# Optimization experiments

Hardware: AMD Instinct MI355X
Metric: run time of the kernel (lower is better)

The kernel has to match this reference:

```python
import jax, jax.numpy as jnp
import numpy as np

VOCAB, HIDDEN, BATCH, T = 32000, 256, 16, 256


def setup_inputs() -> dict:
    key = jax.random.key(0)
    ks = jax.random.split(key, 8)
    s_in = 1.0 / np.sqrt(HIDDEN)  # torch nn.RNN init scale (1/sqrt(hidden))
    inputs = jax.random.randint(ks[0], (BATCH, T), 0, VOCAB)
    targets = jax.random.randint(ks[1], (BATCH, T), 0, VOCAB)
    # RNN params: torch stores W_ih as (hidden, vocab); we keep the transpose
    # (vocab, hidden) so one_hot(x) @ W_ih.T == Wih[x] (an exact gather).
    Wih = jax.random.uniform(ks[2], (VOCAB, HIDDEN), minval=-s_in, maxval=s_in)
    bih = jax.random.uniform(ks[3], (HIDDEN,), minval=-s_in, maxval=s_in)
    Whh = jax.random.uniform(ks[4], (HIDDEN, HIDDEN), minval=-s_in, maxval=s_in)
    bhh = jax.random.uniform(ks[5], (HIDDEN,), minval=-s_in, maxval=s_in)
    Wfc = jax.random.uniform(ks[6], (VOCAB, HIDDEN), minval=-s_in, maxval=s_in)
    bfc = jax.random.uniform(ks[7], (VOCAB,), minval=-s_in, maxval=s_in)
    return {"inputs": inputs, "targets": targets, "Wih": Wih, "bih": bih,
            "Whh": Whh, "bhh": bhh, "Wfc": Wfc, "bfc": bfc}


def reference(inputs, targets, Wih, bih, Whh, bhh, Wfc, bfc):
    # one_hot(inputs) @ W_ih.T + b_ih  ==  Wih[inputs] + bih (exact same math)
    xproj = Wih[inputs] + bih                      # (B, T, H)
    B = inputs.shape[0]
    h0 = jnp.zeros((B, HIDDEN), dtype=Wih.dtype)

    def step(h, xt):
        h = jnp.tanh(xt + h @ Whh.T + bhh)
        return h, h

    _, hs = jax.lax.scan(step, h0, jnp.swapaxes(xproj, 0, 1))  # (T, B, H)
    hs = jnp.swapaxes(hs, 0, 1)                    # (B, T, H)
    logits = hs @ Wfc.T + bfc                      # (B, T, V)
    logp = jax.nn.log_softmax(logits, axis=-1)
    nll = -jnp.take_along_axis(logp, targets[..., None], axis=-1)
    return jnp.mean(nll)                           # scalar cross-entropy loss
```

## Files before the change

kernel.cpp:

```cpp
#include <hip/hip_runtime.h>
#include <hip/hip_bf16.h>
#include <stdint.h>

#define VOCAB 32000
#define HID   256
#define BATCH 16
#define SEQT  256
#define ROWS  (BATCH*SEQT)

typedef __attribute__((ext_vector_type(8))) short bf16x8_t;
typedef __attribute__((ext_vector_type(4))) float f32x4_t;

__device__ __forceinline__ short f2bs(float x) {
    __hip_bfloat16 h = __float2bfloat16(x);
    return *reinterpret_cast<short*>(&h);
}
__device__ __forceinline__ bf16x8_t cvt8(float4 a, float4 b) {
    union { short s[8]; bf16x8_t v; } u;
    u.s[0] = f2bs(a.x); u.s[1] = f2bs(a.y); u.s[2] = f2bs(a.z); u.s[3] = f2bs(a.w);
    u.s[4] = f2bs(b.x); u.s[5] = f2bs(b.y); u.s[6] = f2bs(b.z); u.s[7] = f2bs(b.w);
    return u.v;
}
__device__ __forceinline__ void barrier_lds() {
    asm volatile("s_waitcnt lgkmcnt(0)\n\ts_barrier" ::: "memory");
}
__device__ __forceinline__ float tanh_exp(float x) {
    float e = __builtin_amdgcn_exp2f(x * 2.885390081777927f);
    return fmaf(-2.f, __builtin_amdgcn_rcpf(e + 1.f), 1.f);
}
__device__ __forceinline__ uint32_t pk_bf16(float lo, float hi) {
    uint32_t r;
    asm("v_cvt_pk_bf16_f32 %0, %1, %2" : "=v"(r) : "v"(lo), "v"(hi));
    return r;
}

__global__ __launch_bounds__(256) void xproj_kernel(
    const int* __restrict__ inputs,
    const float* __restrict__ Wih,
    const float* __restrict__ bih,
    const float* __restrict__ bhh,
    const float* __restrict__ Wfc,
    float* __restrict__ xp,
    float* __restrict__ S,
    __hip_bfloat16* __restrict__ Wfcb,
    int do_cvt)
{
    int idx = blockIdx.x * 256 + threadIdx.x;
    int h  = idx & 255;
    int tb = idx >> 8;
    int b  = tb & 15;
    int t  = tb >> 4;
    int id = inputs[b * SEQT + t];
    xp[idx] = Wih[(size_t)id * HID + h] + bih[h] + bhh[h];
    if (idx < ROWS) S[idx] = 0.0f;
    if (do_cvt && idx < (VOCAB * HID / 8)) {
        const float4* p = (const float4*)(Wfc + (size_t)idx * 8);
        *(bf16x8_t*)((short*)Wfcb + (size_t)idx * 8) = cvt8(p[0], p[1]);
    }
}

__global__ __launch_bounds__(512, 1) void rnn_kernel(
    const float* __restrict__ xp,
    const float* __restrict__ Whh,
    __hip_bfloat16* __restrict__ hs)
{
    __shared__ short hbuf[2][16][264];
    const int tid = threadIdx.x;
    const int l = tid & 63, w = tid >> 6;
    const int lr = l & 15, lh = l >> 4;
    const int cm = tid >> 5;
    const int cc = (tid & 31) * 8;
    const int n0 = w * 32 + lr * 2;

    bf16x8_t bfrag[2][8];
#pragma unroll
    for (int nt = 0; nt < 2; nt++) {
#pragma unroll
        for (int ki = 0; ki < 8; ki++) {
            const float4* p = (const float4*)(Whh + (size_t)(n0 + nt) * HID + ki * 32 + lh * 8);
            bfrag[nt][ki] = cvt8(p[0], p[1]);
        }
    }
    for (int i = tid; i < 16 * 264; i += 512) ((short*)hbuf[0])[i] = 0;
    __syncthreads();

    float2 xva[4], xvb[4];
#pragma unroll
    for (int r = 0; r < 4; r++)
        xva[r] = *(const float2*)(xp + (lh * 4 + r) * HID + n0);

    auto step = [&](int SRC, int DST, float2* xv, float2* xn, int t) {
        if (t > 0) {
            bf16x8_t hv = *(const bf16x8_t*)(&hbuf[SRC][cm][cc]);
            *(bf16x8_t*)((short*)hs + (size_t)(t - 1) * (BATCH * HID) + cm * HID + cc) = hv;
        }
        bf16x8_t afr[8];
#pragma unroll
        for (int ki = 0; ki < 8; ki++)
            afr[ki] = *(const bf16x8_t*)(&hbuf[SRC][lr][ki * 32 + lh * 8]);

        f32x4_t a0a = {xv[0].x, xv[1].x, xv[2].x, xv[3].x};
        f32x4_t a1a = {xv[0].y, xv[1].y, xv[2].y, xv[3].y};
        f32x4_t a0b = {0.f, 0.f, 0.f, 0.f};
        f32x4_t a1b = {0.f, 0.f, 0.f, 0.f};
#pragma unroll
        for (int ki = 0; ki < 4; ki++) {
            a0a = __builtin_amdgcn_mfma_f32_16x16x32_bf16(afr[ki],     bfrag[0][ki],     a0a, 0, 0, 0);
            a0b = __builtin_amdgcn_mfma_f32_16x16x32_bf16(afr[ki + 4], bfrag[0][ki + 4], a0b, 0, 0, 0);
            a1a = __builtin_amdgcn_mfma_f32_16x16x32_bf16(afr[ki],     bfrag[1][ki],     a1a, 0, 0, 0);
            a1b = __builtin_amdgcn_mfma_f32_16x16x32_bf16(afr[ki + 4], bfrag[1][ki + 4], a1b, 0, 0, 0);
        }

        if (t + 1 < SEQT) {
            const float* xb = xp + (size_t)(t + 1) * (BATCH * HID);
#pragma unroll
            for (int r = 0; r < 4; r++)
                xn[r] = *(const float2*)(xb + (lh * 4 + r) * HID + n0);
        }

#pragma unroll
        for (int r = 0; r < 4; r++) {
            float v0 = a0a[r] + a0b[r];
            float v1 = a1a[r] + a1b[r];
            uint32_t pk = pk_bf16(tanh_exp(v0), tanh_exp(v1));
            *(uint32_t*)(&hbuf[DST][lh * 4 + r][n0]) = pk;
        }
        barrier_lds();
    };

    for (int t = 0; t < SEQT; t += 2) {
        step(0, 1, xva, xvb, t);
        step(1, 0, xvb, xva, t + 1);
    }
    bf16x8_t hv = *(const bf16x8_t*)(&hbuf[0][cm][cc]);
    *(bf16x8_t*)((short*)hs + (size_t)(SEQT - 1) * (BATCH * HID) + cm * HID + cc) = hv;
}

template <bool BF16B>
__global__ __launch_bounds__(256) void fc_kernel(
    const __hip_bfloat16* __restrict__ hs,
    const void* __restrict__ WfcP,
    const float* __restrict__ bfc,
    const int* __restrict__ targets,
    float* __restrict__ S,
    float* __restrict__ TL)
{
    __shared__ short As[2][4 * 128 * 8];
    __shared__ short Bs[2][4 * 128 * 8];
    __shared__ int tgt[128];

    const int bid = blockIdx.x;
    const int xcd = bid & 7;
    const int j   = bid >> 3;
    const int m_id = j & 31;
    const int n_id = (j >> 5) * 8 + xcd;
    if (n_id >= VOCAB / 128) return;
    const int m0 = m_id * 128, n0 = n_id * 128;

    const int tid = threadIdx.x;
    const int l = tid & 63, w = tid >> 6;
    const int lr = l & 15, lh = l >> 4;
    const int wm = (w >> 1) * 64, wn = (w & 1) * 64;
    const int row = tid & 127, sub = tid >> 7;

    if (tid < 128) {
        int r = m0 + tid;
        tgt[tid] = targets[((r & 15) << 8) | (r >> 4)];
    }

    f32x4_t acc[4][4];
    const f32x4_t z = {0.f, 0.f, 0.f, 0.f};
#pragma unroll
    for (int i = 0; i < 4; i++)
#pragma unroll
        for (int jj = 0; jj < 4; jj++) acc[i][jj] = z;

    const __hip_bfloat16* gA = hs + (size_t)(m0 + row) * HID + sub * 8;
    const __hip_bfloat16* gBb = (const __hip_bfloat16*)WfcP + (size_t)(n0 + row) * HID + sub * 8;
    const float*          gBf = (const float*)WfcP + (size_t)(n0 + row) * HID + sub * 8;

    bf16x8_t rA0, rA1, rB0, rB1;
    float4 rf0a, rf0b, rf1a, rf1b;

    {
        rA0 = *(const bf16x8_t*)(gA);
        rA1 = *(const bf16x8_t*)(gA + 16);
        *(bf16x8_t*)&As[0][(sub * 128 + row) * 8] = rA0;
        *(bf16x8_t*)&As[0][((sub + 2) * 128 + row) * 8] = rA1;
        if (BF16B) {
            rB0 = *(const bf16x8_t*)(gBb);
            rB1 = *(const bf16x8_t*)(gBb + 16);
            *(bf16x8_t*)&Bs[0][(sub * 128 + row) * 8] = rB0;
            *(bf16x8_t*)&Bs[0][((sub + 2) * 128 + row) * 8] = rB1;
        } else {
            const float4* p0 = (const float4*)(gBf);
            const float4* p1 = (const float4*)(gBf + 16);
            *(bf16x8_t*)&Bs[0][(sub * 128 + row) * 8] = cvt8(p0[0], p0[1]);
            *(bf16x8_t*)&Bs[0][((sub + 2) * 128 + row) * 8] = cvt8(p1[0], p1[1]);
        }
    }
    {
        rA0 = *(const bf16x8_t*)(gA + 32);
        rA1 = *(const bf16x8_t*)(gA + 48);
        if (BF16B) {
            rB0 = *(const bf16x8_t*)(gBb + 32);
            rB1 = *(const bf16x8_t*)(gBb + 48);
        } else {
            rf0a = ((const float4*)(gBf + 32))[0]; rf0b = ((const float4*)(gBf + 32))[1];
            rf1a = ((const float4*)(gBf + 48))[0]; rf1b = ((const float4*)(gBf + 48))[1];
        }
    }
    __syncthreads();

    for (int s = 0; s < 8; s++) {
        const int buf = s & 1;
        bf16x8_t a[4], b[4];
#pragma unroll
        for (int mt = 0; mt < 4; mt++)
            a[mt] = *(const bf16x8_t*)&As[buf][(lh * 128 + wm + mt * 16 + lr) * 8];
#pragma unroll
        for (int nt = 0; nt < 4; nt++)
            b[nt] = *(const bf16x8_t*)&Bs[buf][(lh * 128 + wn + nt * 16 + lr) * 8];

        if (s + 1 < 8) {
            *(bf16x8_t*)&As[buf ^ 1][(sub * 128 + row) * 8] = rA0;
            *(bf16x8_t*)&As[buf ^ 1][((sub + 2) * 128 + row) * 8] = rA1;
            if (BF16B) {
                *(bf16x8_t*)&Bs[buf ^ 1][(sub * 128 + row) * 8] = rB0;
                *(bf16x8_t*)&Bs[buf ^ 1][((sub + 2) * 128 + row) * 8] = rB1;
            } else {
                *(bf16x8_t*)&Bs[buf ^ 1][(sub * 128 + row) * 8] = cvt8(rf0a, rf0b);
                *(bf16x8_t*)&Bs[buf ^ 1][((sub + 2) * 128 + row) * 8] = cvt8(rf1a, rf1b);
            }
        }
        if (s + 2 < 8) {
            int k0 = (s + 2) * 32;
            rA0 = *(const bf16x8_t*)(gA + k0);
            rA1 = *(const bf16x8_t*)(gA + k0 + 16);
            if (BF16B) {
                rB0 = *(const bf16x8_t*)(gBb + k0);
                rB1 = *(const bf16x8_t*)(gBb + k0 + 16);
            } else {
                rf0a = ((const float4*)(gBf + k0))[0];      rf0b = ((const float4*)(gBf + k0))[1];
                rf1a = ((const float4*)(gBf + k0 + 16))[0]; rf1b = ((const float4*)(gBf + k0 + 16))[1];
            }
        }
#pragma unroll
        for (int mt = 0; mt < 4; mt++)
#pragma unroll
            for (int nt = 0; nt < 4; nt++)
                acc[mt][nt] = __builtin_amdgcn_mfma_f32_16x16x32_bf16(a[mt], b[nt], acc[mt][nt], 0, 0, 0);
        barrier_lds();
    }

    int tg[16];
#pragma unroll
    for (int i = 0; i < 16; i++)
        tg[i] = tgt[wm + (i >> 2) * 16 + lh * 4 + (i & 3)];

    float rsum[16];
#pragma unroll
    for (int i = 0; i < 16; i++) rsum[i] = 0.f;
#pragma unroll
    for (int nt = 0; nt < 4; nt++) {
        int n = n0 + wn + nt * 16 + lr;
        float bias = bfc[n];
#pragma unroll
        for (int mt = 0; mt < 4; mt++)
#pragma unroll
            for (int r = 0; r < 4; r++) {
                float v = acc[mt][nt][r] + bias;
                rsum[mt * 4 + r] += __expf(v);
                if (tg[mt * 4 + r] == n)
                    TL[m0 + wm + mt * 16 + lh * 4 + r] = v;
            }
    }
#pragma unroll
    for (int m = 1; m < 16; m <<= 1)
#pragma unroll
        for (int i = 0; i < 16; i++) rsum[i] += __shfl_xor(rsum[i], m, 64);
    if (lr == 0) {
#pragma unroll
        for (int i = 0; i < 16; i++) {
            int r = m0 + wm + (i >> 2) * 16 + lh * 4 + (i & 3);
            atomicAdd(&S[r], rsum[i]);
        }
    }
}

__global__ __launch_bounds__(256) void loss_kernel(
    const float* __restrict__ S,
    const float* __restrict__ TL,
    float* __restrict__ out)
{
    int tid = threadIdx.x;
    float p = 0.f;
    for (int i = tid; i < ROWS; i += 256) p += __logf(S[i]) - TL[i];
#pragma unroll
    for (int m = 1; m < 64; m <<= 1) p += __shfl_xor(p, m, 64);
    __shared__ float red[4];
    if ((tid & 63) == 0) red[tid >> 6] = p;
    __syncthreads();
    if (tid == 0)
        out[0] = (red[0] + red[1] + red[2] + red[3]) / (float)ROWS;
}

extern "C" void kernel_launch(void* const* d_in, const int* in_sizes, int n_in,
                              void* d_out, int out_size, void* d_ws, size_t ws_size,
                              hipStream_t stream)
{
    (void)in_sizes; (void)n_in; (void)out_size;
    const int*   inputs  = (const int*)d_in[0];
    const int*   targets = (const int*)d_in[1];
    const float* Wih = (const float*)d_in[2];
    const float* bih = (const float*)d_in[3];
    const float* Whh = (const float*)d_in[4];
    const float* bhh = (const float*)d_in[5];
    const float* Wfc = (const float*)d_in[6];
    const float* bfc = (const float*)d_in[7];

    float* S  = (float*)d_ws;
    float* TL = S + ROWS;
    float* xp = TL + ROWS;
    __hip_bfloat16* hs = (__hip_bfloat16*)(xp + (size_t)SEQT * BATCH * HID);
    __hip_bfloat16* Wfcb = hs + (size_t)ROWS * HID;

    const size_t need = (size_t)(2 * ROWS) * 4 + (size_t)ROWS * HID * 4
                      + (size_t)ROWS * HID * 2 + (size_t)VOCAB * HID * 2;
    const int use_bf16b = (ws_size >= need) ? 1 : 0;

    xproj_kernel<<<(SEQT * BATCH * HID) / 256, 256, 0, stream>>>(
        inputs, Wih, bih, bhh, Wfc, xp, S, Wfcb, use_bf16b);
    rnn_kernel<<<1, 512, 0, stream>>>(xp, Whh, hs);
    if (use_bf16b)
        fc_kernel<true><<<8192, 256, 0, stream>>>(hs, (const void*)Wfcb, bfc, targets, S, TL);
    else
        fc_kernel<false><<<8192, 256, 0, stream>>>(hs, (const void*)Wfc, bfc, targets, S, TL);
    loss_kernel<<<1, 256, 0, stream>>>(S, TL, (float*)d_out);
}
```

Baseline: 426.8 us.

## Pre-swizzle hs and Wfc into MFMA fragment layout, drop LDS staging in FC GEMM

The RNN kernel now writes hidden states, and the conversion kernel writes bf16 Wfc, in a tiled layout that matches the 16x16x32 MFMA operand fragment order. The FC kernel then loads A and B fragments straight from global memory into registers with a two-slot register double buffer, with no LDS tiles and no per-step barriers. This removes LDS write/read traffic and synchronisation in the GEMM. In exchange, each wave reads its operands from global/L2 on its own, so data is no longer shared through LDS between waves, which raises cache traffic and register pressure.

```diff
diff --git a/kernel.cpp b/kernel.cpp
--- a/kernel.cpp
+++ b/kernel.cpp
@@ -33,6 +33,7 @@
     asm("v_cvt_pk_bf16_f32 %0, %1, %2" : "=v"(r) : "v"(lo), "v"(hi));
     return r;
 }
+
 
 __global__ __launch_bounds__(256) void xproj_kernel(
     const int* __restrict__ inputs,
@@ -55,7 +56,12 @@
     if (idx < ROWS) S[idx] = 0.0f;
     if (do_cvt && idx < (VOCAB * HID / 8)) {
         const float4* p = (const float4*)(Wfc + (size_t)idx * 8);
-        *(bf16x8_t*)((short*)Wfcb + (size_t)idx * 8) = cvt8(p[0], p[1]);
+        int n  = idx >> 5;
+        int c  = idx & 31;
+        int ki = c >> 2;
+        int lh = c & 3;
+        size_t dst = (size_t)(n >> 4) * 4096 + ki * 512 + lh * 128 + (n & 15) * 8;
+        *(bf16x8_t*)((short*)Wfcb + dst) = cvt8(p[0], p[1]);
     }
 }
 
@@ -71,6 +77,7 @@
     const int cm = tid >> 5;
     const int cc = (tid & 31) * 8;
     const int n0 = w * 32 + lr * 2;
+    const int cpoff = ((cc >> 5) * 512) + (((cc >> 3) & 3) * 128) + cm * 8;
 
     bf16x8_t bfrag[2][8];
 #pragma unroll
@@ -92,7 +99,7 @@
     auto step = [&](int SRC, int DST, float2* xv, float2* xn, int t) {
         if (t > 0) {
             bf16x8_t hv = *(const bf16x8_t*)(&hbuf[SRC][cm][cc]);
-            *(bf16x8_t*)((short*)hs + (size_t)(t - 1) * (BATCH * HID) + cm * HID + cc) = hv;
+            *(bf16x8_t*)((short*)hs + (size_t)(t - 1) * 4096 + cpoff) = hv;
         }
         bf16x8_t afr[8];
 #pragma unroll
@@ -133,20 +140,18 @@
         step(1, 0, xvb, xva, t + 1);
     }
     bf16x8_t hv = *(const bf16x8_t*)(&hbuf[0][cm][cc]);
-    *(bf16x8_t*)((short*)hs + (size_t)(SEQT - 1) * (BATCH * HID) + cm * HID + cc) = hv;
+    *(bf16x8_t*)((short*)hs + (size_t)(SEQT - 1) * 4096 + cpoff) = hv;
 }
 
 template <bool BF16B>
 __global__ __launch_bounds__(256) void fc_kernel(
-    const __hip_bfloat16* __restrict__ hs,
+    const __hip_bfloat16* __restrict__ hsz,
     const void* __restrict__ WfcP,
     const float* __restrict__ bfc,
     const int* __restrict__ targets,
     float* __restrict__ S,
     float* __restrict__ TL)
 {
-    __shared__ short As[2][4 * 128 * 8];
-    __shared__ short Bs[2][4 * 128 * 8];
     __shared__ int tgt[128];
 
     const int bid = blockIdx.x;
@@ -161,13 +166,18 @@
     const int l = tid & 63, w = tid >> 6;
     const int lr = l & 15, lh = l >> 4;
     const int wm = (w >> 1) * 64, wn = (w & 1) * 64;
-    const int row = tid & 127, sub = tid >> 7;
 
     if (tid < 128) {
         int r = m0 + tid;
         tgt[tid] = targets[((r & 15) << 8) | (r >> 4)];
     }
 
+    const short* Ab = (const short*)hsz +
+        ((size_t)(m_id * 8 + (wm >> 4)) * 8) * 512 + l * 8;
+    const short* Bb = (const short*)WfcP +
+        ((size_t)(n_id * 8 + (wn >> 4)) * 8) * 512 + l * 8;
+    const float* Bf = (const float*)WfcP;
+
     f32x4_t acc[4][4];
     const f32x4_t z = {0.f, 0.f, 0.f, 0.f};
 #pragma unroll
@@ -175,83 +185,38 @@
 #pragma unroll
         for (int jj = 0; jj < 4; jj++) acc[i][jj] = z;
 
-    const __hip_bfloat16* gA = hs + (size_t)(m0 + row) * HID + sub * 8;
-    const __hip_bfloat16* gBb = (const __hip_bfloat16*)WfcP + (size_t)(n0 + row) * HID + sub * 8;
-    const float*          gBf = (const float*)WfcP + (size_t)(n0 + row) * HID + sub * 8;
-
-    bf16x8_t rA0, rA1, rB0, rB1;
-    float4 rf0a, rf0b, rf1a, rf1b;
-
-    {
-        rA0 = *(const bf16x8_t*)(gA);
-        rA1 = *(const bf16x8_t*)(gA + 16);
-        *(bf16x8_t*)&As[0][(sub * 128 + row) * 8] = rA0;
-        *(bf16x8_t*)&As[0][((sub + 2) * 128 + row) * 8] = rA1;
-        if (BF16B) {
-            rB0 = *(const bf16x8_t*)(gBb);
-            rB1 = *(const bf16x8_t*)(gBb + 16);
-            *(bf16x8_t*)&Bs[0][(sub * 128 + row) * 8] = rB0;
-            *(bf16x8_t*)&Bs[0][((sub + 2) * 128 + row) * 8] = rB1;
-        } else {
-            const float4* p0 = (const float4*)(gBf);
-            const float4* p1 = (const float4*)(gBf + 16);
-            *(bf16x8_t*)&Bs[0][(sub * 128 + row) * 8] = cvt8(p0[0], p0[1]);
-            *(bf16x8_t*)&Bs[0][((sub + 2) * 128 + row) * 8] = cvt8(p1[0], p1[1]);
-        }
-    }
-    {
-        rA0 = *(const bf16x8_t*)(gA + 32);
-        rA1 = *(const bf16x8_t*)(gA + 48);
-        if (BF16B) {
-            rB0 = *(const bf16x8_t*)(gBb + 32);
-            rB1 = *(const bf16x8_t*)(gBb + 48);
-        } else {
-            rf0a = ((const float4*)(gBf + 32))[0]; rf0b = ((const float4*)(gBf + 32))[1];
-            rf1a = ((const float4*)(gBf + 48))[0]; rf1b = ((const float4*)(gBf + 48))[1];
-        }
+    bf16x8_t a[2][4], b[2][4];
+    auto loadA = [&](int buf, int ki) {
+#pragma unroll
+        for (int mt = 0; mt < 4; mt++)
+            a[buf][mt] = *(const bf16x8_t*)(Ab + mt * 4096 + ki * 512);
+    };
+    auto loadB = [&](int buf, int ki) {
+#pragma unroll
+        for (int nt = 0; nt < 4; nt++) {
+            if (BF16B) {
+                b[buf][nt] = *(const bf16x8_t*)(Bb + nt * 4096 + ki * 512);
+            } else {
+                int n = n0 + wn + nt * 16 + lr;
+                const float4* p = (const float4*)(Bf + (size_t)n * HID + ki * 32 + lh * 8);
+                b[buf][nt] = cvt8(p[0], p[1]);
+            }
+        }
+    };
+
+    loadA(0, 0); loadB(0, 0);
+#pragma unroll
+    for (int ki = 0; ki < 8; ki++) {
+        const int cur = ki & 1;
+        if (ki < 7) { loadA(cur ^ 1, ki + 1); loadB(cur ^ 1, ki + 1); }
+#pragma unroll
+        for (int mt = 0; mt < 4; mt++)
+#pragma unroll
+            for (int nt = 0; nt < 4; nt++)
+                acc[mt][nt] = __builtin_amdgcn_mfma_f32_16x16x32_bf16(
+                    a[cur][mt], b[cur][nt], acc[mt][nt], 0, 0, 0);
     }
     __syncthreads();
-
-    for (int s = 0; s < 8; s++) {
-        const int buf = s & 1;
-        bf16x8_t a[4], b[4];
-#pragma unroll
-        for (int mt = 0; mt < 4; mt++)
-            a[mt] = *(const bf16x8_t*)&As[buf][(lh * 128 + wm + mt * 16 + lr) * 8];
-#pragma unroll
-        for (int nt = 0; nt < 4; nt++)
-            b[nt] = *(const bf16x8_t*)&Bs[buf][(lh * 128 + wn + nt * 16 + lr) * 8];
-
-        if (s + 1 < 8) {
-            *(bf16x8_t*)&As[buf ^ 1][(sub * 128 + row) * 8] = rA0;
-            *(bf16x8_t*)&As[buf ^ 1][((sub + 2) * 128 + row) * 8] = rA1;
-            if (BF16B) {
-                *(bf16x8_t*)&Bs[buf ^ 1][(sub * 128 + row) * 8] = rB0;
-                *(bf16x8_t*)&Bs[buf ^ 1][((sub + 2) * 128 + row) * 8] = rB1;
-            } else {
-                *(bf16x8_t*)&Bs[buf ^ 1][(sub * 128 + row) * 8] = cvt8(rf0a, rf0b);
-                *(bf16x8_t*)&Bs[buf ^ 1][((sub + 2) * 128 + row) * 8] = cvt8(rf1a, rf1b);
-            }
-        }
-        if (s + 2 < 8) {
-            int k0 = (s + 2) * 32;
-            rA0 = *(const bf16x8_t*)(gA + k0);
-            rA1 = *(const bf16x8_t*)(gA + k0 + 16);
-            if (BF16B) {
-                rB0 = *(const bf16x8_t*)(gBb + k0);
-                rB1 = *(const bf16x8_t*)(gBb + k0 + 16);
-            } else {
-                rf0a = ((const float4*)(gBf + k0))[0];      rf0b = ((const float4*)(gBf + k0))[1];
-                rf1a = ((const float4*)(gBf + k0 + 16))[0]; rf1b = ((const float4*)(gBf + k0 + 16))[1];
-            }
-        }
-#pragma unroll
-        for (int mt = 0; mt < 4; mt++)
-#pragma unroll
-            for (int nt = 0; nt < 4; nt++)
-                acc[mt][nt] = __builtin_amdgcn_mfma_f32_16x16x32_bf16(a[mt], b[nt], acc[mt][nt], 0, 0, 0);
-        barrier_lds();
-    }
 
     int tg[16];
 #pragma unroll
```

Result: slower. 468.0 us (+9.7%).
